# Kernel optimization log

Hardware: AMD Instinct MI355X
Metric: run time of the kernel (lower is better)

The kernel has to match this reference:

```python
import jax, jax.numpy as jnp
import numpy as np
from jax import lax

T, B, IN, H, OUT = 2048, 128, 2, 200, 1


def setup_inputs() -> dict:
    key = jax.random.key(0)
    ks = jax.random.split(key, 7)
    s_ih = 1.0 / np.sqrt(H)
    return {
        "input_seq": jax.random.normal(ks[0], (T, B, IN), dtype=jnp.float32),
        "W_ih": jax.random.normal(ks[1], (H, IN), dtype=jnp.float32) * s_ih,
        "W_hh": jax.random.normal(ks[2], (H, H), dtype=jnp.float32) * s_ih,
        "b_ih": jax.random.normal(ks[3], (H,), dtype=jnp.float32) * s_ih,
        "b_hh": jax.random.normal(ks[4], (H,), dtype=jnp.float32) * s_ih,
        "W_out": jax.random.normal(ks[5], (OUT, H), dtype=jnp.float32) * s_ih,
        "b_out": jax.random.normal(ks[6], (OUT,), dtype=jnp.float32) * s_ih,
    }


def reference(input_seq, W_ih, W_hh, b_ih, b_hh, W_out, b_out):
    # torch.nn.RNN (tanh, 1 layer, seq-first): h_t = tanh(x_t W_ih^T + b_ih + h_{t-1} W_hh^T + b_hh)
    # Precompute the input projection for all timesteps (vectorized), fold both biases.
    x_proj = jnp.einsum('tbi,hi->tbh', input_seq, W_ih) + (b_ih + b_hh)  # [T,B,H]

    def step(h, xt):
        h_new = jnp.tanh(xt + h @ W_hh.T)
        return h_new, h_new

    h0 = jnp.zeros((input_seq.shape[1], W_hh.shape[0]), dtype=input_seq.dtype)
    _, hs = lax.scan(step, h0, x_proj)  # hs: [T,B,H]
    # Final linear head applied to every timestep output
    return jnp.einsum('tbh,oh->tbo', hs, W_out) + b_out  # [T,B,1]
```

## Files before the change

kernel.cpp:

```cpp
#include <hip/hip_runtime.h>
#include <hip/hip_fp16.h>


typedef short s8v __attribute__((ext_vector_type(8)));
typedef short s4v __attribute__((ext_vector_type(4)));
typedef float f4v __attribute__((ext_vector_type(4)));

static constexpr int T = 2048;
static constexpr int B = 128;
static constexpr int H = 200;
static constexpr int NTHR = 1024;
static constexpr int NT  = 13;
static constexpr int KT  = 7;
static constexpr int HP  = 224;
static constexpr int RS  = 8;

__device__ __forceinline__ unsigned short f2h(float f) {
    const __half h = __float2half_rn(f);
    return *(const unsigned short*)&h;
}
__device__ __forceinline__ float h2f(unsigned short u) {
    const __half h = *(const __half*)&u;
    return __half2float(h);
}
template <int CTRL>
__device__ __forceinline__ float dpp_add(float v) {
    const int i = __builtin_bit_cast(int, v);
    const int p = __builtin_amdgcn_update_dpp(0, i, CTRL, 0xF, 0xF, false);
    return v + __builtin_bit_cast(float, p);
}

__global__ __attribute__((amdgpu_flat_work_group_size(NTHR, NTHR),
                          amdgpu_waves_per_eu(4, 4)))
void rnn_fused(const float* __restrict__ x,
               const float* __restrict__ W_ih,
               const float* __restrict__ W_hh,
               const float* __restrict__ b_ih,
               const float* __restrict__ b_hh,
               const float* __restrict__ W_out,
               const float* __restrict__ b_out,
               float* __restrict__ out)
{
    const int b    = blockIdx.x;
    const int tid  = threadIdx.x;
    const int w    = tid >> 6;
    const int lane = tid & 63;
    const int m    = lane & 15;
    const int q    = lane >> 4;

    const bool hasT = (w < NT);
    const int  nA   = 16 * w + m;
    const bool colv = hasT && (nA < H);

    __shared__ __align__(16) unsigned short ring[RS][2][HP];
    __shared__ __align__(16) float xs[2 * T];
    __shared__ __align__(16) float obuf[128];

    for (int i = tid; i < RS * 2 * HP; i += NTHR) (&ring[0][0][0])[i] = 0;
    for (int idx = tid; idx < T; idx += NTHR) {
        const float2 v = *(const float2*)(x + (size_t)idx * (B * 2) + 2 * b);
        xs[2 * idx] = v.x; xs[2 * idx + 1] = v.y;
    }

    s8v BA[KT];
#pragma unroll
    for (int kt = 0; kt < KT; ++kt) {
        s8v ba{};
        if (colv) {
#pragma unroll
            for (int j = 0; j < 8; ++j) {
                const int ks = 32 * kt + 8 * q + j;
                ba[j] = (short)((ks < H) ? f2h(W_hh[nA * H + ks])
                                         : (unsigned short)0);
            }
        }
        BA[kt] = ba;
    }

    const float wxA0 = colv ? W_ih[nA * 2]     : 0.f;
    const float wxA1 = colv ? W_ih[nA * 2 + 1] : 0.f;
    const float bA   = colv ? (b_ih[nA] + b_hh[nA]) : 0.f;

    const int c4 = 4 * lane;
    f4v wo = {0.f, 0.f, 0.f, 0.f};
    if (c4 + 3 < H) wo = *(const f4v*)(W_out + c4);
    const float bo = b_out[0];

    __syncthreads();

    float* const op = out + b;
    const unsigned short* const aptr = &ring[0][(m == 1) ? 1 : 0][8 * q];

    auto drain = [&](int slot, int tout) {
        float v = 0.f;
        if (lane < 56) {
            const s4v hv = *(const s4v*)(&ring[slot][0][0] + c4);
            const s4v lv = *(const s4v*)(&ring[slot][1][0] + c4);
            v = (h2f((unsigned short)hv[0]) + h2f((unsigned short)lv[0])) * wo[0]
              + (h2f((unsigned short)hv[1]) + h2f((unsigned short)lv[1])) * wo[1]
              + (h2f((unsigned short)hv[2]) + h2f((unsigned short)lv[2])) * wo[2]
              + (h2f((unsigned short)hv[3]) + h2f((unsigned short)lv[3])) * wo[3];
        }
        v = dpp_add<0xB1>(v);
        v = dpp_add<0x4E>(v);
        v = dpp_add<0x141>(v);
        v = dpp_add<0x140>(v);
        const float r1 = __builtin_bit_cast(float,
            __builtin_amdgcn_readlane(__builtin_bit_cast(int, v), 16));
        const float r2 = __builtin_bit_cast(float,
            __builtin_amdgcn_readlane(__builtin_bit_cast(int, v), 32));
        const float r3 = __builtin_bit_cast(float,
            __builtin_amdgcn_readlane(__builtin_bit_cast(int, v), 48));
        if (lane == 0) obuf[tout & 127] = ((v + r1) + (r2 + r3)) + bo;
    };

    for (int t8 = 0; t8 < T / RS; ++t8) {
        f4v xv0 = {0.f, 0.f, 0.f, 0.f};
        f4v xv1 = {0.f, 0.f, 0.f, 0.f};
#pragma unroll
        for (int rp = 0; rp < RS; ++rp) {
            const int t  = 8 * t8 + rp;
            const int sr = (rp + RS - 1) & (RS - 1);

            if (hasT) {
                if (rp == 0) {
                    xv0 = *(const f4v*)(xs + 16 * t8);
                    xv1 = *(const f4v*)(xs + 16 * t8 + 4);
                } else if (rp == 4) {
                    xv0 = *(const f4v*)(xs + 16 * t8 + 8);
                    xv1 = *(const f4v*)(xs + 16 * t8 + 12);
                }
                const int r2i = rp & 3;
                const float x0 = (r2i == 0) ? xv0[0] : (r2i == 1) ? xv0[2]
                               : (r2i == 2) ? xv1[0] : xv1[2];
                const float x1 = (r2i == 0) ? xv0[1] : (r2i == 1) ? xv0[3]
                               : (r2i == 2) ? xv1[1] : xv1[3];
                const float xterm = fmaf(x0, wxA0, fmaf(x1, wxA1, bA));

                const unsigned short* ap = aptr + sr * 448;
                const s8v A0 = *(const s8v*)(ap);
                const s8v A1 = *(const s8v*)(ap + 32);
                const s8v A2 = *(const s8v*)(ap + 64);
                const s8v A3 = *(const s8v*)(ap + 96);
                const s8v A4 = *(const s8v*)(ap + 128);
                const s8v A5 = *(const s8v*)(ap + 160);
                const s8v A6 = *(const s8v*)(ap + 192);

                f4v u0 = {0.f, 0.f, 0.f, 0.f};
                f4v u1 = {0.f, 0.f, 0.f, 0.f};
                f4v u2 = {0.f, 0.f, 0.f, 0.f};
                f4v u3 = {0.f, 0.f, 0.f, 0.f};
                u0 = __builtin_amdgcn_mfma_f32_16x16x32_f16(A0, BA[0], u0, 0, 0, 0);
                u1 = __builtin_amdgcn_mfma_f32_16x16x32_f16(A2, BA[2], u1, 0, 0, 0);
                u2 = __builtin_amdgcn_mfma_f32_16x16x32_f16(A4, BA[4], u2, 0, 0, 0);
                u3 = __builtin_amdgcn_mfma_f32_16x16x32_f16(A6, BA[6], u3, 0, 0, 0);
                u0 = __builtin_amdgcn_mfma_f32_16x16x32_f16(A1, BA[1], u0, 0, 0, 0);
                u1 = __builtin_amdgcn_mfma_f32_16x16x32_f16(A3, BA[3], u1, 0, 0, 0);
                u2 = __builtin_amdgcn_mfma_f32_16x16x32_f16(A5, BA[5], u2, 0, 0, 0);

                if (q == 0 && nA < H) {
                    const float y = ((u0[0] + u0[1]) + (u1[0] + u1[1]))
                                  + ((u2[0] + u2[1]) + (u3[0] + u3[1]));
                    const float pre = y + xterm;
                    const float e   = __expf(2.f * pre);
                    const float th  = 1.f - 2.f / (e + 1.f);
                    const unsigned short hi = f2h(th);
                    (&ring[rp][0][0])[nA] = hi;
                    (&ring[rp][1][0])[nA] = f2h(th - h2f(hi));
                }
            } else if (w == 13 + (rp & 1)) {
                if (t8 > 0 || rp >= 2) drain((rp + 6) & (RS - 1), t - 2);
            } else if (w == 15) {
                if (rp == 0 && (t8 & 7) == 2 && t8 >= 10) {
                    const int cc = (t8 - 10) >> 3;
                    const float val = obuf[((cc & 1) << 6) | lane];
                    op[(size_t)(64 * cc + lane) * B] = val;
                }
            }
            __syncthreads();
        }
    }

    if (w == 13) drain(6, 2046);
    if (w == 14) drain(7, 2047);
    __syncthreads();
    if (w == 15) {
        const float val = obuf[64 | lane];
        op[(size_t)(1984 + lane) * B] = val;
    }
}

extern "C" void kernel_launch(void* const* d_in, const int* in_sizes, int n_in,
                              void* d_out, int out_size, void* d_ws, size_t ws_size,
                              hipStream_t stream) {
    const float* x     = (const float*)d_in[0];
    const float* W_ih  = (const float*)d_in[1];
    const float* W_hh  = (const float*)d_in[2];
    const float* b_ih  = (const float*)d_in[3];
    const float* b_hh  = (const float*)d_in[4];
    const float* W_out = (const float*)d_in[5];
    const float* b_out = (const float*)d_in[6];
    float* out = (float*)d_out;

    rnn_fused<<<B, NTHR, 0, stream>>>(x, W_ih, W_hh, b_ih, b_hh, W_out, b_out, out);
}
```

Measured before the change: 1.010 ms.

## Move the last eight hidden columns to VALU tail waves and fold the tanh scale into the weights

The MFMA-wave count drops from 13 to 12, so the MFMA waves cover hidden columns 0-191. The remaining 8 columns (192-199) are now computed by two new tail waves using VALU FMAs plus DPP and readlane reductions. This removes the mostly-empty 13th MFMA wave, and the drain and output roles are reassigned to waves 12 and 13. Separately, the factor 2·log2(e) is folded into W_hh, W_ih and the biases so tanh uses exp2 directly, saving one multiply per step. The risk is that the tail waves' longer reduction chain, with its serial readlanes, becomes the per-step critical path before each barrier, and scaling W_hh before the fp16 conversion slightly changes rounding.

```diff
diff --git a/kernel.cpp b/kernel.cpp
--- a/kernel.cpp
+++ b/kernel.cpp
@@ -10,10 +10,11 @@
 static constexpr int B = 128;
 static constexpr int H = 200;
 static constexpr int NTHR = 1024;
-static constexpr int NT  = 13;
+static constexpr int NT  = 12;
 static constexpr int KT  = 7;
 static constexpr int HP  = 224;
 static constexpr int RS  = 8;
+static constexpr float C2L = 2.8853900817779268f;
 
 __device__ __forceinline__ unsigned short f2h(float f) {
     const __half h = __float2half_rn(f);
@@ -28,6 +29,10 @@
     const int i = __builtin_bit_cast(int, v);
     const int p = __builtin_amdgcn_update_dpp(0, i, CTRL, 0xF, 0xF, false);
     return v + __builtin_bit_cast(float, p);
+}
+__device__ __forceinline__ float rlane(float v, int l) {
+    return __builtin_bit_cast(float,
+        __builtin_amdgcn_readlane(__builtin_bit_cast(int, v), l));
 }
 
 __global__ __attribute__((amdgpu_flat_work_group_size(NTHR, NTHR),
@@ -48,9 +53,10 @@
     const int m    = lane & 15;
     const int q    = lane >> 4;
 
-    const bool hasT = (w < NT);
+    const bool hasT   = (w < NT);
+    const bool isTail = (w >= 14);
     const int  nA   = 16 * w + m;
-    const bool colv = hasT && (nA < H);
+    const bool colv = hasT;
 
     __shared__ __align__(16) unsigned short ring[RS][2][HP];
     __shared__ __align__(16) float xs[2 * T];
@@ -70,18 +76,41 @@
 #pragma unroll
             for (int j = 0; j < 8; ++j) {
                 const int ks = 32 * kt + 8 * q + j;
-                ba[j] = (short)((ks < H) ? f2h(W_hh[nA * H + ks])
+                ba[j] = (short)((ks < H) ? f2h(C2L * W_hh[nA * H + ks])
                                          : (unsigned short)0);
             }
         }
         BA[kt] = ba;
     }
 
-    const float wxA0 = colv ? W_ih[nA * 2]     : 0.f;
-    const float wxA1 = colv ? W_ih[nA * 2 + 1] : 0.f;
-    const float bA   = colv ? (b_ih[nA] + b_hh[nA]) : 0.f;
+    const float wxA0 = colv ? (C2L * W_ih[nA * 2])     : 0.f;
+    const float wxA1 = colv ? (C2L * W_ih[nA * 2 + 1]) : 0.f;
+    const float bA   = colv ? (C2L * (b_ih[nA] + b_hh[nA])) : 0.f;
 
     const int c4 = 4 * lane;
+    float tw0[4] = {0,0,0,0}, tw1[4] = {0,0,0,0};
+    float tw2[4] = {0,0,0,0}, tw3[4] = {0,0,0,0};
+    float twx0 = 0.f, twx1 = 0.f, tbA = 0.f;
+    if (isTail) {
+        const int cb = 192 + 4 * (w - 14);
+#pragma unroll
+        for (int j = 0; j < 4; ++j) {
+            const int k = c4 + j;
+            if (lane < 56 && k < H) {
+                tw0[j] = h2f(f2h(C2L * W_hh[(cb + 0) * H + k]));
+                tw1[j] = h2f(f2h(C2L * W_hh[(cb + 1) * H + k]));
+                tw2[j] = h2f(f2h(C2L * W_hh[(cb + 2) * H + k]));
+                tw3[j] = h2f(f2h(C2L * W_hh[(cb + 3) * H + k]));
+            }
+        }
+        if (lane < 4) {
+            const int c = cb + lane;
+            twx0 = C2L * W_ih[c * 2];
+            twx1 = C2L * W_ih[c * 2 + 1];
+            tbA  = C2L * (b_ih[c] + b_hh[c]);
+        }
+    }
+
     f4v wo = {0.f, 0.f, 0.f, 0.f};
     if (c4 + 3 < H) wo = *(const f4v*)(W_out + c4);
     const float bo = b_out[0];
@@ -105,12 +134,9 @@
         v = dpp_add<0x4E>(v);
         v = dpp_add<0x141>(v);
         v = dpp_add<0x140>(v);
-        const float r1 = __builtin_bit_cast(float,
-            __builtin_amdgcn_readlane(__builtin_bit_cast(int, v), 16));
-        const float r2 = __builtin_bit_cast(float,
-            __builtin_amdgcn_readlane(__builtin_bit_cast(int, v), 32));
-        const float r3 = __builtin_bit_cast(float,
-            __builtin_amdgcn_readlane(__builtin_bit_cast(int, v), 48));
+        const float r1 = rlane(v, 16);
+        const float r2 = rlane(v, 32);
+        const float r3 = rlane(v, 48);
         if (lane == 0) obuf[tout & 127] = ((v + r1) + (r2 + r3)) + bo;
     };
 
@@ -122,7 +148,7 @@
             const int t  = 8 * t8 + rp;
             const int sr = (rp + RS - 1) & (RS - 1);
 
-            if (hasT) {
+            if (hasT || isTail) {
                 if (rp == 0) {
                     xv0 = *(const f4v*)(xs + 16 * t8);
                     xv1 = *(const f4v*)(xs + 16 * t8 + 4);
@@ -130,11 +156,14 @@
                     xv0 = *(const f4v*)(xs + 16 * t8 + 8);
                     xv1 = *(const f4v*)(xs + 16 * t8 + 12);
                 }
-                const int r2i = rp & 3;
-                const float x0 = (r2i == 0) ? xv0[0] : (r2i == 1) ? xv0[2]
-                               : (r2i == 2) ? xv1[0] : xv1[2];
-                const float x1 = (r2i == 0) ? xv0[1] : (r2i == 1) ? xv0[3]
-                               : (r2i == 2) ? xv1[1] : xv1[3];
+            }
+            const int r2i = rp & 3;
+            const float x0 = (r2i == 0) ? xv0[0] : (r2i == 1) ? xv0[2]
+                           : (r2i == 2) ? xv1[0] : xv1[2];
+            const float x1 = (r2i == 0) ? xv0[1] : (r2i == 1) ? xv0[3]
+                           : (r2i == 2) ? xv1[1] : xv1[3];
+
+            if (hasT) {
                 const float xterm = fmaf(x0, wxA0, fmaf(x1, wxA1, bA));
 
                 const unsigned short* ap = aptr + sr * 448;
@@ -158,19 +187,57 @@
                 u1 = __builtin_amdgcn_mfma_f32_16x16x32_f16(A3, BA[3], u1, 0, 0, 0);
                 u2 = __builtin_amdgcn_mfma_f32_16x16x32_f16(A5, BA[5], u2, 0, 0, 0);
 
-                if (q == 0 && nA < H) {
+                if (q == 0) {
                     const float y = ((u0[0] + u0[1]) + (u1[0] + u1[1]))
                                   + ((u2[0] + u2[1]) + (u3[0] + u3[1]));
                     const float pre = y + xterm;
-                    const float e   = __expf(2.f * pre);
-                    const float th  = 1.f - 2.f / (e + 1.f);
+                    const float e2  = __builtin_amdgcn_exp2f(pre);
+                    const float th  = 1.f - 2.f / (e2 + 1.f);
                     const unsigned short hi = f2h(th);
                     (&ring[rp][0][0])[nA] = hi;
                     (&ring[rp][1][0])[nA] = f2h(th - h2f(hi));
                 }
-            } else if (w == 13 + (rp & 1)) {
+            } else if (isTail) {
+                float v0 = 0.f, v1 = 0.f, v2 = 0.f, v3 = 0.f;
+                if (lane < 56) {
+                    const s4v hv = *(const s4v*)(&ring[sr][0][0] + c4);
+                    const s4v lv = *(const s4v*)(&ring[sr][1][0] + c4);
+#pragma unroll
+                    for (int j = 0; j < 4; ++j) {
+                        const float hs = h2f((unsigned short)hv[j])
+                                       + h2f((unsigned short)lv[j]);
+                        v0 = fmaf(hs, tw0[j], v0);
+                        v1 = fmaf(hs, tw1[j], v1);
+                        v2 = fmaf(hs, tw2[j], v2);
+                        v3 = fmaf(hs, tw3[j], v3);
+                    }
+                }
+                v0 = dpp_add<0xB1>(v0);  v1 = dpp_add<0xB1>(v1);
+                v2 = dpp_add<0xB1>(v2);  v3 = dpp_add<0xB1>(v3);
+                v0 = dpp_add<0x4E>(v0);  v1 = dpp_add<0x4E>(v1);
+                v2 = dpp_add<0x4E>(v2);  v3 = dpp_add<0x4E>(v3);
+                v0 = dpp_add<0x141>(v0); v1 = dpp_add<0x141>(v1);
+                v2 = dpp_add<0x141>(v2); v3 = dpp_add<0x141>(v3);
+                v0 = dpp_add<0x140>(v0); v1 = dpp_add<0x140>(v1);
+                v2 = dpp_add<0x140>(v2); v3 = dpp_add<0x140>(v3);
+                const float t0 = ((v0 + rlane(v0, 16)) + (rlane(v0, 32) + rlane(v0, 48)));
+                const float t1 = ((v1 + rlane(v1, 16)) + (rlane(v1, 32) + rlane(v1, 48)));
+                const float t2 = ((v2 + rlane(v2, 16)) + (rlane(v2, 32) + rlane(v2, 48)));
+                const float t3 = ((v3 + rlane(v3, 16)) + (rlane(v3, 32) + rlane(v3, 48)));
+                if (lane < 4) {
+                    const float ytot = (lane == 0) ? t0 : (lane == 1) ? t1
+                                     : (lane == 2) ? t2 : t3;
+                    const float pre = ytot + fmaf(x0, twx0, fmaf(x1, twx1, tbA));
+                    const float e2  = __builtin_amdgcn_exp2f(pre);
+                    const float th  = 1.f - 2.f / (e2 + 1.f);
+                    const unsigned short hi = f2h(th);
+                    const int c = 192 + 4 * (w - 14) + lane;
+                    (&ring[rp][0][0])[c] = hi;
+                    (&ring[rp][1][0])[c] = f2h(th - h2f(hi));
+                }
+            } else if (w == 12 + (rp & 1)) {
                 if (t8 > 0 || rp >= 2) drain((rp + 6) & (RS - 1), t - 2);
-            } else if (w == 15) {
+            } else if (w == 13) {
                 if (rp == 0 && (t8 & 7) == 2 && t8 >= 10) {
                     const int cc = (t8 - 10) >> 3;
                     const float val = obuf[((cc & 1) << 6) | lane];
@@ -181,8 +248,8 @@
         }
     }
 
-    if (w == 13) drain(6, 2046);
-    if (w == 14) drain(7, 2047);
+    if (w == 12) drain(6, 2046);
+    if (w == 13) drain(7, 2047);
     __syncthreads();
     if (w == 15) {
         const float val = obuf[64 | lane];
```

Measured after the change: 1.328 ms. 31.5% more time.
